# Kernel optimization log

Measured on AMD Instinct MI355X. Metric: run time of the kernel, lower is better.

The kernel has to match this reference:

```python
import jax, jax.numpy as jnp
import numpy as np

S, B, H = 4096, 128, 128
D_WIN = 2.0
SIGMA = D_WIN / 2.0


def setup_inputs() -> dict:
    key = jax.random.key(0)
    k1, k2, k3, k4, k5, k6 = jax.random.split(key, 6)
    return {
        "e": jax.random.normal(k1, (S, B, H), dtype=jnp.float32),
        "d": jax.random.normal(k2, (1, B, H), dtype=jnp.float32),
        "W_a": jax.random.normal(k3, (H, H), dtype=jnp.float32),
        "W_p": jax.random.normal(k4, (H, H), dtype=jnp.float32),
        "v_p": jax.random.normal(k5, (H, 1), dtype=jnp.float32),
        "W_c": jax.random.normal(k6, (2 * H, H), dtype=jnp.float32),
    }


def reference(e, d, W_a, W_p, v_p, W_c):
    s = e.shape[0]
    # alignment: scores over source positions, softmax along S (dim 0)
    scores = jnp.einsum('sbh,sbh->sb', e, jnp.broadcast_to(d @ W_a, e.shape))  # [S,B]
    a = jax.nn.softmax(scores, axis=0)
    # predictive position p_t in [0, S]
    p_t = (s * jax.nn.sigmoid(jnp.tanh(d @ W_p) @ v_p)).squeeze()  # [B]
    pos = jnp.arange(s, dtype=e.dtype)[:, None]                    # [S,1]
    diff = p_t[None, :] - pos                                      # [S,B]
    mask = (jnp.abs(diff) <= D_WIN).astype(e.dtype)
    gauss = jnp.exp(-(diff ** 2) / (2.0 * SIGMA ** 2)) * mask
    w = a * gauss                                                  # [S,B]
    context = jnp.einsum('sbh,sb->bh', e, w)[None]                 # [1,B,H]
    x = jnp.concatenate([context, d], axis=2)                      # [1,B,2H]
    output = jnp.tanh(x @ W_c)                                     # [1,B,H]
    return output, w
```

## Files before the change

### kernel.cpp

```cpp
#include <hip/hip_runtime.h>
#include <math.h>

#define S_DIM 4096
#define B_DIM 128
#define H_DIM 128
#define NBLK  32
#define CHUNK (S_DIM / NBLK)
#define NEG_BIG -1e30f

__global__ __launch_bounds__(256) void k_prep(
    const float* __restrict__ d, const float* __restrict__ Wa,
    const float* __restrict__ Wp, const float* __restrict__ vp,
    float* __restrict__ dWa, float* __restrict__ pt)
{
    int b  = blockIdx.x;
    int t  = threadIdx.x;
    int h  = t & 127;
    int kh = t >> 7;
    __shared__ float db[H_DIM];
    if (t < H_DIM) db[t] = d[b * H_DIM + t];
    __syncthreads();
    float aa = 0.f, ap = 0.f;
    int k0 = kh * 64;
    #pragma unroll 8
    for (int k = k0; k < k0 + 64; ++k) {
        float dk = db[k];
        aa = fmaf(dk, Wa[k * H_DIM + h], aa);
        ap = fmaf(dk, Wp[k * H_DIM + h], ap);
    }
    __shared__ float paa[256], pap[256];
    paa[t] = aa; pap[t] = ap;
    __syncthreads();
    if (t < H_DIM) {
        float a2 = paa[t] + paa[t + 128];
        float p2 = pap[t] + pap[t + 128];
        dWa[b * H_DIM + t] = a2;
        float r = tanhf(p2) * vp[t];
        #pragma unroll
        for (int o = 1; o < 64; o <<= 1) r += __shfl_xor(r, o);
        __shared__ float red[2];
        if ((t & 63) == 0) red[t >> 6] = r;
        __syncthreads();
        if (t == 0) {
            float sum = red[0] + red[1];
            pt[b] = (float)S_DIM / (1.f + __expf(-sum));
        }
    }
}

__global__ __launch_bounds__(256) void k_scores(
    const float* __restrict__ e, const float* __restrict__ dWa,
    const float* __restrict__ pt,
    float* __restrict__ pm, float* __restrict__ pl, float* __restrict__ win)
{
    int b    = blockIdx.x;
    int blk  = blockIdx.y;
    int tid  = threadIdx.x;
    int wave = tid >> 6;
    int lane = tid & 63;
    int half = lane >> 5;
    int hl   = lane & 31;
    int halfIdx = wave * 2 + half;

    float4 wf = ((const float4*)(dWa + b * H_DIM))[hl];
    float ptb = pt[b];
    int   s0  = (int)floorf(ptb) - 2;

    int sbase = blk * CHUNK + halfIdx;
    const float* ep = e + (size_t)sbase * (B_DIM * H_DIM) + b * H_DIM + hl * 4;
    const size_t stride8 = (size_t)8 * B_DIM * H_DIM;

    float4 ev[16];
    #pragma unroll
    for (int j = 0; j < 16; ++j)
        ev[j] = *(const float4*)(ep + (size_t)j * stride8);

    float v[16];
    #pragma unroll
    for (int j = 0; j < 16; ++j)
        v[j] = ev[j].x * wf.x + ev[j].y * wf.y + ev[j].z * wf.z + ev[j].w * wf.w;

    #pragma unroll
    for (int o = 1; o < 32; o <<= 1) {
        #pragma unroll
        for (int j = 0; j < 16; ++j)
            v[j] += __shfl_xor(v[j], o);
    }

    float M = v[0];
    #pragma unroll
    for (int j = 1; j < 16; ++j) M = fmaxf(M, v[j]);
    float L = 0.f;
    #pragma unroll
    for (int j = 0; j < 16; ++j) L += __expf(v[j] - M);

    if (hl == 0) {
        #pragma unroll
        for (int j = 0; j < 16; ++j) {
            int s = sbase + 8 * j;
            int idx = s - s0;
            if (idx >= 0 && idx < 5) {
                float diff = ptb - (float)s;
                if (fabsf(diff) <= 2.0f) win[b * 5 + idx] = v[j];
            }
        }
    }

    __shared__ float ms[8], ls[8];
    if (hl == 0) { ms[halfIdx] = M; ls[halfIdx] = L; }
    __syncthreads();
    if (tid == 0) {
        float Mb = NEG_BIG;
        #pragma unroll
        for (int j = 0; j < 8; ++j) Mb = fmaxf(Mb, ms[j]);
        float Lb = 0.f;
        #pragma unroll
        for (int j = 0; j < 8; ++j) Lb += ls[j] * __expf(ms[j] - Mb);
        pm[b * NBLK + blk] = Mb;
        pl[b * NBLK + blk] = Lb;
    }
}

__global__ __launch_bounds__(256) void k_final(
    const float* __restrict__ e, const float* __restrict__ d,
    const float* __restrict__ Wc,
    const float* __restrict__ pm, const float* __restrict__ pl,
    const float* __restrict__ win, const float* __restrict__ pt,
    float* __restrict__ out)
{
    int b = blockIdx.x;
    int t = threadIdx.x;

    __shared__ float sh[2];
    __shared__ float wv[5];
    __shared__ float x[2 * H_DIM];
    __shared__ float part[2][H_DIM];

    if (t < 64) {
        float m = (t < NBLK) ? pm[b * NBLK + t] : NEG_BIG;
        float l = (t < NBLK) ? pl[b * NBLK + t] : 0.f;
        float M = m;
        #pragma unroll
        for (int o = 1; o < 64; o <<= 1) M = fmaxf(M, __shfl_xor(M, o));
        float ls = l * __expf(m - M);
        #pragma unroll
        for (int o = 1; o < 64; o <<= 1) ls += __shfl_xor(ls, o);
        if (t == 0) { sh[0] = M; sh[1] = ls; }
    }
    __syncthreads();
    float M = sh[0], L = sh[1];
    float ptb = pt[b];
    int   s0  = (int)floorf(ptb) - 2;

    if (t < 5) {
        int s = s0 + t;
        float v = 0.f;
        if (s >= 0 && s < S_DIM) {
            float diff = ptb - (float)s;
            if (fabsf(diff) <= 2.0f) {
                v = __expf(win[b * 5 + t] - M) / L * __expf(-0.5f * diff * diff);
                out[B_DIM * H_DIM + (size_t)s * B_DIM + b] = v;
            }
        }
        wv[t] = v;
    }
    __syncthreads();

    if (t < H_DIM) {
        float ctx = 0.f;
        #pragma unroll
        for (int k = 0; k < 5; ++k) {
            int s = s0 + k;
            if (s >= 0 && s < S_DIM)
                ctx = fmaf(wv[k], e[(size_t)s * (B_DIM * H_DIM) + b * H_DIM + t], ctx);
        }
        x[t] = ctx;
    } else {
        x[t] = d[b * H_DIM + (t - H_DIM)];
    }
    __syncthreads();

    int h  = t & 127;
    int jh = t >> 7;
    float acc = 0.f;
    int j0 = jh * H_DIM;
    #pragma unroll 8
    for (int j = j0; j < j0 + H_DIM; ++j)
        acc = fmaf(x[j], Wc[j * H_DIM + h], acc);
    part[jh][h] = acc;
    __syncthreads();
    if (t < H_DIM)
        out[b * H_DIM + t] = tanhf(part[0][t] + part[1][t]);
}

extern "C" void kernel_launch(void* const* d_in, const int* in_sizes, int n_in,
                              void* d_out, int out_size, void* d_ws, size_t ws_size,
                              hipStream_t stream)
{
    const float* e  = (const float*)d_in[0];
    const float* d  = (const float*)d_in[1];
    const float* Wa = (const float*)d_in[2];
    const float* Wp = (const float*)d_in[3];
    const float* vp = (const float*)d_in[4];
    const float* Wc = (const float*)d_in[5];
    float* out = (float*)d_out;

    float* ws  = (float*)d_ws;
    float* dWa = ws;
    float* pt  = ws + 16384;
    float* pm  = ws + 16512;
    float* pl  = ws + 20608;
    float* win = ws + 24704;

    hipMemsetAsync(out + B_DIM * H_DIM, 0, (size_t)S_DIM * B_DIM * sizeof(float), stream);

    k_prep  <<<B_DIM, 256, 0, stream>>>(d, Wa, Wp, vp, dWa, pt);
    k_scores<<<dim3(B_DIM, NBLK), 256, 0, stream>>>(e, dWa, pt, pm, pl, win);
    k_final <<<B_DIM, 256, 0, stream>>>(e, d, Wc, pm, pl, win, pt, out);
}
```

Measured before the change: 381.3 us.

## Stream contiguous e rows per block and merge many softmax partials in final

The score kernel now gives each block 4 full contiguous S rows (all B and H) instead of one batch column over a strided S chunk, so global reads are fully contiguous and issued through a rolling 8-deep register prefetch. Per-row scores go to shared memory, and each block writes per-batch max and sum partials over its 4 rows. That yields 1024 partials per batch, which k_final merges with an online-softmax reduction across 256 threads and four waves. The aim is better DRAM streaming efficiency for the 256MB e read, at the cost of more partial traffic, a dWa reload per row, and a heavier final reduction.

```diff
diff --git a/kernel.cpp b/kernel.cpp
--- a/kernel.cpp
+++ b/kernel.cpp
@@ -4,8 +4,8 @@
 #define S_DIM 4096
 #define B_DIM 128
 #define H_DIM 128
-#define NBLK  32
-#define CHUNK (S_DIM / NBLK)
+#define ROWS  4
+#define NBLK  (S_DIM / ROWS)
 #define NEG_BIG -1e30f
 
 __global__ __launch_bounds__(256) void k_prep(
@@ -53,71 +53,56 @@
     const float* __restrict__ pt,
     float* __restrict__ pm, float* __restrict__ pl, float* __restrict__ win)
 {
-    int b    = blockIdx.x;
-    int blk  = blockIdx.y;
-    int tid  = threadIdx.x;
-    int wave = tid >> 6;
-    int lane = tid & 63;
-    int half = lane >> 5;
-    int hl   = lane & 31;
-    int halfIdx = wave * 2 + half;
-
-    float4 wf = ((const float4*)(dWa + b * H_DIM))[hl];
-    float ptb = pt[b];
-    int   s0  = (int)floorf(ptb) - 2;
-
-    int sbase = blk * CHUNK + halfIdx;
-    const float* ep = e + (size_t)sbase * (B_DIM * H_DIM) + b * H_DIM + hl * 4;
-    const size_t stride8 = (size_t)8 * B_DIM * H_DIM;
-
-    float4 ev[16];
+    int blk = blockIdx.x;
+    int t   = threadIdx.x;
+    int hl  = t & 31;
+    int hi  = t >> 5;
+
+    __shared__ float sc[ROWS][B_DIM + 1];
+
+    const float4* ebase = (const float4*)e + (size_t)blk * (ROWS * B_DIM * H_DIM / 4) + t;
+
+    float4 ev[8];
     #pragma unroll
-    for (int j = 0; j < 16; ++j)
-        ev[j] = *(const float4*)(ep + (size_t)j * stride8);
-
-    float v[16];
-    #pragma unroll
-    for (int j = 0; j < 16; ++j)
-        v[j] = ev[j].x * wf.x + ev[j].y * wf.y + ev[j].z * wf.z + ev[j].w * wf.w;
-
-    #pragma unroll
-    for (int o = 1; o < 32; o <<= 1) {
-        #pragma unroll
-        for (int j = 0; j < 16; ++j)
-            v[j] += __shfl_xor(v[j], o);
-    }
-
-    float M = v[0];
-    #pragma unroll
-    for (int j = 1; j < 16; ++j) M = fmaxf(M, v[j]);
-    float L = 0.f;
-    #pragma unroll
-    for (int j = 0; j < 16; ++j) L += __expf(v[j] - M);
-
-    if (hl == 0) {
-        #pragma unroll
-        for (int j = 0; j < 16; ++j) {
-            int s = sbase + 8 * j;
+    for (int j = 0; j < 8; ++j)
+        ev[j] = ebase[(size_t)j * 256];
+
+    #pragma unroll 16
+    for (int j = 0; j < 64; ++j) {
+        float4 cur = ev[j & 7];
+        if (j + 8 < 64) ev[j & 7] = ebase[(size_t)(j + 8) * 256];
+        int b = ((j & 15) << 3) + hi;
+        float4 wf = ((const float4*)(dWa + (b << 7)))[hl];
+        float v = cur.x * wf.x + cur.y * wf.y + cur.z * wf.z + cur.w * wf.w;
+        v += __shfl_xor(v, 1);
+        v += __shfl_xor(v, 2);
+        v += __shfl_xor(v, 4);
+        v += __shfl_xor(v, 8);
+        v += __shfl_xor(v, 16);
+        if (hl == 0) sc[j >> 4][b] = v;
+    }
+    __syncthreads();
+
+    if (t < B_DIM) {
+        int b = t;
+        float r0 = sc[0][b], r1 = sc[1][b], r2 = sc[2][b], r3 = sc[3][b];
+        float M = fmaxf(fmaxf(r0, r1), fmaxf(r2, r3));
+        float L = __expf(r0 - M) + __expf(r1 - M) + __expf(r2 - M) + __expf(r3 - M);
+        pm[(size_t)b * NBLK + blk] = M;
+        pl[(size_t)b * NBLK + blk] = L;
+
+        float ptb = pt[b];
+        int   s0  = (int)floorf(ptb) - 2;
+        float rv[ROWS] = {r0, r1, r2, r3};
+        #pragma unroll
+        for (int i = 0; i < ROWS; ++i) {
+            int s = blk * ROWS + i;
             int idx = s - s0;
             if (idx >= 0 && idx < 5) {
                 float diff = ptb - (float)s;
-                if (fabsf(diff) <= 2.0f) win[b * 5 + idx] = v[j];
+                if (fabsf(diff) <= 2.0f) win[b * 5 + idx] = rv[i];
             }
         }
-    }
-
-    __shared__ float ms[8], ls[8];
-    if (hl == 0) { ms[halfIdx] = M; ls[halfIdx] = L; }
-    __syncthreads();
-    if (tid == 0) {
-        float Mb = NEG_BIG;
-        #pragma unroll
-        for (int j = 0; j < 8; ++j) Mb = fmaxf(Mb, ms[j]);
-        float Lb = 0.f;
-        #pragma unroll
-        for (int j = 0; j < 8; ++j) Lb += ls[j] * __expf(ms[j] - Mb);
-        pm[b * NBLK + blk] = Mb;
-        pl[b * NBLK + blk] = Lb;
     }
 }
 
@@ -135,17 +120,35 @@
     __shared__ float wv[5];
     __shared__ float x[2 * H_DIM];
     __shared__ float part[2][H_DIM];
-
-    if (t < 64) {
-        float m = (t < NBLK) ? pm[b * NBLK + t] : NEG_BIG;
-        float l = (t < NBLK) ? pl[b * NBLK + t] : 0.f;
-        float M = m;
-        #pragma unroll
-        for (int o = 1; o < 64; o <<= 1) M = fmaxf(M, __shfl_xor(M, o));
-        float ls = l * __expf(m - M);
-        #pragma unroll
-        for (int o = 1; o < 64; o <<= 1) ls += __shfl_xor(ls, o);
-        if (t == 0) { sh[0] = M; sh[1] = ls; }
+    __shared__ float wm[4], wl[4];
+
+    {
+        float m = NEG_BIG, l = 0.f;
+        #pragma unroll
+        for (int k = 0; k < 4; ++k) {
+            float mm = pm[(size_t)b * NBLK + t + 256 * k];
+            float ll = pl[(size_t)b * NBLK + t + 256 * k];
+            float M2 = fmaxf(m, mm);
+            l = l * __expf(m - M2) + ll * __expf(mm - M2);
+            m = M2;
+        }
+        #pragma unroll
+        for (int o = 1; o < 64; o <<= 1) {
+            float mo = __shfl_xor(m, o);
+            float lo = __shfl_xor(l, o);
+            float M2 = fmaxf(m, mo);
+            l = l * __expf(m - M2) + lo * __expf(mo - M2);
+            m = M2;
+        }
+        if ((t & 63) == 0) { wm[t >> 6] = m; wl[t >> 6] = l; }
+        __syncthreads();
+        if (t == 0) {
+            float M2 = fmaxf(fmaxf(wm[0], wm[1]), fmaxf(wm[2], wm[3]));
+            float L2 = 0.f;
+            #pragma unroll
+            for (int j = 0; j < 4; ++j) L2 += wl[j] * __expf(wm[j] - M2);
+            sh[0] = M2; sh[1] = L2;
+        }
     }
     __syncthreads();
     float M = sh[0], L = sh[1];
@@ -209,12 +212,12 @@
     float* dWa = ws;
     float* pt  = ws + 16384;
     float* pm  = ws + 16512;
-    float* pl  = ws + 20608;
-    float* win = ws + 24704;
+    float* pl  = ws + 147584;
+    float* win = ws + 278656;
 
     hipMemsetAsync(out + B_DIM * H_DIM, 0, (size_t)S_DIM * B_DIM * sizeof(float), stream);
 
     k_prep  <<<B_DIM, 256, 0, stream>>>(d, Wa, Wp, vp, dWa, pt);
-    k_scores<<<dim3(B_DIM, NBLK), 256, 0, stream>>>(e, dWa, pt, pm, pl, win);
+    k_scores<<<NBLK, 256, 0, stream>>>(e, dWa, pt, pm, pl, win);
     k_final <<<B_DIM, 256, 0, stream>>>(e, d, Wc, pm, pl, win, pt, out);
 }
```

Result: slower. 389.3 us (+2.1%).
